# Optimization experiments

Measured on AMD Instinct MI355X. Metric: run time of the kernel, lower is better.

## Reference

```python
import jax, jax.numpy as jnp
import numpy as np

HIDDEN = 3072
N_HEADS = 24
N_KV = 8
HEAD_DIM = HIDDEN // N_HEADS          # 128
ROT = int(HEAD_DIM * 0.75)            # 96 (partial rotary)
OP_SIZE = N_HEADS * HEAD_DIM + 2 * N_KV * HEAD_DIM  # 5120
LORA_R = 256
LORA_SCALE = 512.0 / LORA_R           # 2.0
ROPE_THETA = 10000.0
SCALE = HEAD_DIM ** -0.5


def setup_inputs() -> dict:
    key = jax.random.key(0)
    ks = jax.random.split(key, 8)
    B, S = 2, 2048
    hidden_states = jax.random.normal(ks[0], (B, S, HIDDEN), dtype=jnp.float32)
    position_ids = jnp.arange(B * S, dtype=jnp.int64 if jax.config.jax_enable_x64 else jnp.int32).reshape(B, S)
    w = lambda k, o, i: jax.random.normal(k, (o, i), dtype=jnp.float32) * (i ** -0.5)
    return {
        "hidden_states": hidden_states,
        "Wqkv": w(ks[1], OP_SIZE, HIDDEN),
        "Aqkv": w(ks[2], LORA_R, HIDDEN),
        "Bqkv": w(ks[3], OP_SIZE, LORA_R) * 0.01,
        "Wo": w(ks[4], HIDDEN, N_HEADS * HEAD_DIM),
        "Ao": w(ks[5], LORA_R, N_HEADS * HEAD_DIM),
        "Bo": w(ks[6], HIDDEN, LORA_R) * 0.01,
        "position_ids": position_ids,
    }


def _lora_linear(x, W, A, Bm):
    # base GEMM + low-rank LoRA update, scaling = alpha/r
    return x @ W.T + (x @ A.T) @ Bm.T * LORA_SCALE


def _rotate_half(x):
    h = x.shape[-1] // 2
    return jnp.concatenate((-x[..., h:], x[..., :h]), axis=-1)


def reference(hidden_states, Wqkv, Aqkv, Bqkv, Wo, Ao, Bo, position_ids):
    B, S, _ = hidden_states.shape
    qkv = _lora_linear(hidden_states, Wqkv, Aqkv, Bqkv)  # [B,S,5120]
    q_pos = N_HEADS * HEAD_DIM
    kv_pos = N_KV * HEAD_DIM
    q = qkv[..., :q_pos].reshape(B, S, N_HEADS, HEAD_DIM)
    k = qkv[..., q_pos:q_pos + kv_pos].reshape(B, S, N_KV, HEAD_DIM)
    v = qkv[..., q_pos + kv_pos:].reshape(B, S, N_KV, HEAD_DIM)

    # partial RoPE: cos/sin cache over rotary_ndims=96
    inv_freq = 1.0 / (ROPE_THETA ** (jnp.arange(0, ROT, 2, dtype=jnp.float32) / ROT))  # [48]
    freqs = position_ids.astype(jnp.float32)[..., None] * inv_freq  # [B,S,48]
    emb = jnp.concatenate((freqs, freqs), axis=-1)                   # [B,S,96]
    cos = jnp.cos(emb)[:, :, None, :]  # broadcast over head axis (bsnd)
    sin = jnp.sin(emb)[:, :, None, :]

    def rope(x):
        xr, xp = x[..., :ROT], x[..., ROT:]
        xr = xr * cos + _rotate_half(xr) * sin
        return jnp.concatenate((xr, xp), axis=-1)

    q = rope(q)
    k = rope(k)

    # GQA: repeat kv heads to match query heads
    groups = N_HEADS // N_KV
    k = jnp.repeat(k, groups, axis=2)
    v = jnp.repeat(v, groups, axis=2)

    scores = jnp.einsum('bqhd,bkhd->bhqk', q, k) * SCALE  # [B,H,S,S]
    causal = jnp.tril(jnp.ones((S, S), dtype=bool))
    scores = jnp.where(causal, scores, jnp.finfo(scores.dtype).min)
    probs = jax.nn.softmax(scores, axis=-1)
    attn = jnp.einsum('bhqk,bkhd->bqhd', probs, v).reshape(B, S, N_HEADS * HEAD_DIM)
    return _lora_linear(attn, Wo, Ao, Bo)
```

## Files before the change

### kernel.cpp

```cpp
#include <hip/hip_runtime.h>

typedef unsigned short u16;
typedef unsigned int   u32;

typedef __bf16 bf16_t;
typedef bf16_t bf16x8 __attribute__((ext_vector_type(8)));
typedef float  f32x4  __attribute__((ext_vector_type(4)));
typedef float  f32x16 __attribute__((ext_vector_type(16)));
typedef u16    u16x8  __attribute__((ext_vector_type(8)));
typedef u32    u32x4  __attribute__((ext_vector_type(4)));

__device__ __forceinline__ float bf2f(u16 u) { return __uint_as_float(((u32)u) << 16); }
__device__ __forceinline__ u16 f2bf(float f) {
  u32 u = __float_as_uint(f);
  u32 r = u + 0x7fffu + ((u >> 16) & 1u);
  return (u16)(r >> 16);
}
__device__ __forceinline__ float fast_exp2(float x) { return __builtin_amdgcn_exp2f(x); }

__device__ __forceinline__ void gload_lds16(const u16* g, u16* l) {
  __builtin_amdgcn_global_load_lds(
      (const __attribute__((address_space(1))) void*)g,
      (__attribute__((address_space(3))) void*)l,
      16, 0, 0);
}

#define SBAR0() __builtin_amdgcn_sched_barrier(0)
#define HWBAR() __builtin_amdgcn_s_barrier()

__global__ void k_cast_all(const float* __restrict__ x,  const float* __restrict__ wq,
                           const float* __restrict__ bq, const float* __restrict__ aq,
                           const float* __restrict__ wo, const float* __restrict__ bo,
                           const float* __restrict__ ao,
                           u16* __restrict__ xw, u16* __restrict__ wwq, u16* __restrict__ aqkvb,
                           u16* __restrict__ wwo, u16* __restrict__ aob) {
  const int total = 5177344;
  int i = blockIdx.x * blockDim.x + threadIdx.x;
  const int stride = gridDim.x * blockDim.x;
  for (; i < total; i += stride) {
    const float* src; u16* dst; int r, c8, L, off, sL;
    if (i < 1572864)      { int loc = i;           r = loc / 384; c8 = loc - r * 384; src = x;  dst = xw;    L = 3328; off = 0;    sL = 3072; }
    else if (i < 3538944) { int loc = i - 1572864; r = loc / 384; c8 = loc - r * 384; src = wq; dst = wwq;   L = 3328; off = 0;    sL = 3072; }
    else if (i < 3702784) { int loc = i - 3538944; r = loc >> 5;  c8 = loc & 31;      src = bq; dst = wwq;   L = 3328; off = 3072; sL = 256;  }
    else if (i < 3801088) { int loc = i - 3702784; r = loc / 384; c8 = loc - r * 384; src = aq; dst = aqkvb; L = 3072; off = 0;    sL = 3072; }
    else if (i < 4980736) { int loc = i - 3801088; r = loc / 384; c8 = loc - r * 384; src = wo; dst = wwo;   L = 3328; off = 0;    sL = 3072; }
    else if (i < 5079040) { int loc = i - 4980736; r = loc >> 5;  c8 = loc & 31;      src = bo; dst = wwo;   L = 3328; off = 3072; sL = 256;  }
    else                  { int loc = i - 5079040; r = loc / 384; c8 = loc - r * 384; src = ao; dst = aob;   L = 3072; off = 0;    sL = 3072; }
    const f32x4* p = (const f32x4*)(src + (size_t)r * sL + c8 * 8);
    f32x4 a = p[0], b2 = p[1];
    u16x8 o;
    o[0] = f2bf(a[0]);  o[1] = f2bf(a[1]);  o[2] = f2bf(a[2]);  o[3] = f2bf(a[3]);
    o[4] = f2bf(b2[0]); o[5] = f2bf(b2[1]); o[6] = f2bf(b2[2]); o[7] = f2bf(b2[3]);
    *(u16x8*)(dst + (size_t)r * L + off + c8 * 8) = o;
  }
}

__global__ void k_red4_cast(const float* __restrict__ t4, u16* __restrict__ out,
                            int C8, int L, int off, float scale, size_t plane) {
  const int r  = blockIdx.y;
  const int c8 = blockIdx.x * 64 + threadIdx.x;
  if (c8 >= C8) return;
  size_t base = (size_t)r * (C8 * 8) + c8 * 8;
  float s[8];
#pragma unroll
  for (int j = 0; j < 8; ++j) s[j] = 0.f;
#pragma unroll
  for (int p = 0; p < 4; ++p) {
    const f32x4* q = (const f32x4*)(t4 + p * plane + base);
    f32x4 a = q[0], b = q[1];
    s[0] += a[0]; s[1] += a[1]; s[2] += a[2]; s[3] += a[3];
    s[4] += b[0]; s[5] += b[1]; s[6] += b[2]; s[7] += b[3];
  }
  u16x8 o;
#pragma unroll
  for (int j = 0; j < 8; ++j) o[j] = f2bf(s[j] * scale);
  *(u16x8*)(out + (size_t)r * L + off + c8 * 8) = o;
}

__global__ __launch_bounds__(256) void k_gemm_bt_sk(
    const u16* __restrict__ A, const u16* __restrict__ B, float* __restrict__ C,
    int M, int N, int lda, int ldb, int kc) {
  __shared__ u16 As[64][64 + 8];
  __shared__ u16 Bs[64][64 + 8];
  const int tid   = threadIdx.x;
  const int lane  = tid & 63;
  const int w     = tid >> 6;
  const int wm    = (w >> 1) * 32;
  const int wn    = (w & 1) * 32;
  const int row16 = lane & 15;
  const int quad  = lane >> 4;
  const int m0 = blockIdx.y * 64;
  const int n0 = blockIdx.x * 64;
  const int ldr = tid >> 2;
  const int ldc = (tid & 3) * 16;
  const int z   = blockIdx.z;
  float* Cz = C + (size_t)z * M * N;
  const int kbeg = z * kc, kend = kbeg + kc;

  f32x4 acc[2][2] = {};

  for (int k0 = kbeg; k0 < kend; k0 += 64) {
    const u16* ga = A + (size_t)(m0 + ldr) * lda + (k0 + ldc);
    const u16* gb = B + (size_t)(n0 + ldr) * ldb + (k0 + ldc);
    u16x8 a0 = *(const u16x8*)ga;
    u16x8 a1 = *(const u16x8*)(ga + 8);
    u16x8 b0 = *(const u16x8*)gb;
    u16x8 b1 = *(const u16x8*)(gb + 8);
    __syncthreads();
    *(u16x8*)&As[ldr][ldc]     = a0;
    *(u16x8*)&As[ldr][ldc + 8] = a1;
    *(u16x8*)&Bs[ldr][ldc]     = b0;
    *(u16x8*)&Bs[ldr][ldc + 8] = b1;
    __syncthreads();
#pragma unroll
    for (int kk = 0; kk < 64; kk += 32) {
      bf16x8 af0 = *(const bf16x8*)&As[wm + row16][kk + quad * 8];
      bf16x8 af1 = *(const bf16x8*)&As[wm + 16 + row16][kk + quad * 8];
      bf16x8 bg0 = *(const bf16x8*)&Bs[wn + row16][kk + quad * 8];
      bf16x8 bg1 = *(const bf16x8*)&Bs[wn + 16 + row16][kk + quad * 8];
      acc[0][0] = __builtin_amdgcn_mfma_f32_16x16x32_bf16(af0, bg0, acc[0][0], 0, 0, 0);
      acc[0][1] = __builtin_amdgcn_mfma_f32_16x16x32_bf16(af0, bg1, acc[0][1], 0, 0, 0);
      acc[1][0] = __builtin_amdgcn_mfma_f32_16x16x32_bf16(af1, bg0, acc[1][0], 0, 0, 0);
      acc[1][1] = __builtin_amdgcn_mfma_f32_16x16x32_bf16(af1, bg1, acc[1][1], 0, 0, 0);
    }
  }
#pragma unroll
  for (int tm = 0; tm < 2; ++tm)
#pragma unroll
    for (int tn = 0; tn < 2; ++tn) {
      int gm = m0 + wm + tm * 16 + quad * 4;
      int gn = n0 + wn + tn * 16 + row16;
#pragma unroll
      for (int r = 0; r < 4; ++r)
        Cz[(size_t)(gm + r) * N + gn] = acc[tm][tn][r];
    }
}

__device__ __forceinline__ void stage_half(
    int H, int nt4,
    const u16* __restrict__ A, const u16* __restrict__ B, int S,
    int m0, int n0, u16* AsB, u16* BsB,
    int w, int rowin, int colsw) {
  if (H >= nt4) return;
  const int t = H >> 2, slot = H & 3;
  const int half = slot & 1;
  const u16* G = (slot < 2) ? A : B;
  const int r0 = (slot < 2) ? m0 : n0;
  u16* lds = ((slot < 2) ? AsB : BsB) + (t & 1) * 16384 + half * 8192;
  const int k0 = t * 64;
#pragma unroll
  for (int i = 0; i < 2; ++i) {
    const int chunk = w * 2 + i;
    const int row = half * 128 + chunk * 8 + rowin;
    gload_lds16(G + (size_t)(r0 + row) * S + k0 + colsw, lds + chunk * 512);
  }
}

__device__ __forceinline__ bf16x8 frag_ld(const u16* base, int row, int c16) {
  return *(const bf16x8*)(base + row * 64 + ((c16 ^ (row & 7)) << 3));
}

template <int RB>
__device__ __forceinline__ void gemm256_group(
    int k, int nt,
    const u16* __restrict__ A, const u16* __restrict__ B, int S,
    int m0, int n0, u16* AsB, u16* BsB,
    int wr, int wc, int row16, int quad, int w, int rowin, int colsw,
    f32x4 (&acc)[8][4]) {
  const u16* Ab = AsB + RB * 16384;
  const u16* Bb = BsB + RB * 16384;
  const int nt4 = nt * 4;
  bf16x8 a0[4][2], a1[4][2], b0[2][2], b1[2][2];

#pragma unroll
  for (int mf = 0; mf < 4; ++mf)
#pragma unroll
    for (int kk = 0; kk < 2; ++kk)
      a0[mf][kk] = frag_ld(Ab, wr * 128 + mf * 16 + row16, kk * 4 + quad);
#pragma unroll
  for (int nf = 0; nf < 2; ++nf)
#pragma unroll
    for (int kk = 0; kk < 2; ++kk)
      b0[nf][kk] = frag_ld(Bb, wc * 64 + nf * 16 + row16, kk * 4 + quad);
  stage_half(4 * k + 5, nt4, A, B, S, m0, n0, AsB, BsB, w, rowin, colsw);
  SBAR0(); HWBAR(); SBAR0();
  __builtin_amdgcn_s_setprio(1);
#pragma unroll
  for (int mf = 0; mf < 4; ++mf)
#pragma unroll
    for (int nf = 0; nf < 2; ++nf)
#pragma unroll
      for (int kk = 0; kk < 2; ++kk)
        acc[mf][nf] = __builtin_amdgcn_mfma_f32_16x16x32_bf16(a0[mf][kk], b0[nf][kk], acc[mf][nf], 0, 0, 0);
  __builtin_amdgcn_s_setprio(0);
  SBAR0(); HWBAR(); SBAR0();

#pragma unroll
  for (int nf = 0; nf < 2; ++nf)
#pragma unroll
    for (int kk = 0; kk < 2; ++kk)
      b1[nf][kk] = frag_ld(Bb, wc * 64 + 32 + nf * 16 + row16, kk * 4 + quad);
  stage_half(4 * k + 6, nt4, A, B, S, m0, n0, AsB, BsB, w, rowin, colsw);
  SBAR0(); HWBAR(); SBAR0();
  __builtin_amdgcn_s_setprio(1);
#pragma unroll
  for (int mf = 0; mf < 4; ++mf)
#pragma unroll
    for (int nf = 0; nf < 2; ++nf)
#pragma unroll
      for (int kk = 0; kk < 2; ++kk)
        acc[mf][2 + nf] = __builtin_amdgcn_mfma_f32_16x16x32_bf16(a0[mf][kk], b1[nf][kk], acc[mf][2 + nf], 0, 0, 0);
  __builtin_amdgcn_s_setprio(0);
  SBAR0(); HWBAR(); SBAR0();

#pragma unroll
  for (int mf = 0; mf < 4; ++mf)
#pragma unroll
    for (int kk = 0; kk < 2; ++kk)
      a1[mf][kk] = frag_ld(Ab, wr * 128 + 64 + mf * 16 + row16, kk * 4 + quad);
  stage_half(4 * k + 7, nt4, A, B, S, m0, n0, AsB, BsB, w, rowin, colsw);
  SBAR0(); HWBAR(); SBAR0();
  __builtin_amdgcn_s_setprio(1);
#pragma unroll
  for (int mf = 0; mf < 4; ++mf)
#pragma unroll
    for (int nf = 0; nf < 2; ++nf)
#pragma unroll
      for (int kk = 0; kk < 2; ++kk)
        acc[4 + mf][nf] = __builtin_amdgcn_mfma_f32_16x16x32_bf16(a1[mf][kk], b0[nf][kk], acc[4 + mf][nf], 0, 0, 0);
  __builtin_amdgcn_s_setprio(0);
  SBAR0(); HWBAR(); SBAR0();

  stage_half(4 * k + 8, nt4, A, B, S, m0, n0, AsB, BsB, w, rowin, colsw);
  SBAR0();
  if (k < nt - 2) { asm volatile("s_waitcnt vmcnt(2)" ::: "memory"); }
  else            { asm volatile("s_waitcnt vmcnt(0)" ::: "memory"); }
  HWBAR(); SBAR0();
  __builtin_amdgcn_s_setprio(1);
#pragma unroll
  for (int mf = 0; mf < 4; ++mf)
#pragma unroll
    for (int nf = 0; nf < 2; ++nf)
#pragma unroll
      for (int kk = 0; kk < 2; ++kk)
        acc[4 + mf][2 + nf] = __builtin_amdgcn_mfma_f32_16x16x32_bf16(a1[mf][kk], b1[nf][kk], acc[4 + mf][2 + nf], 0, 0, 0);
  __builtin_amdgcn_s_setprio(0);
  SBAR0(); HWBAR(); SBAR0();
}

template <int ATOMIC>
__device__ __forceinline__ void gemm256_run(
    const u16* __restrict__ A, const u16* __restrict__ B, int S, int nt,
    int m0, int n0, float* __restrict__ C, int ldc, int cn0,
    u16* As, u16* Bs) {
  const int tid   = threadIdx.x;
  const int lane  = tid & 63;
  const int w     = tid >> 6;
  const int wr    = w >> 2;
  const int wc    = w & 3;
  const int row16 = lane & 15;
  const int quad  = lane >> 4;
  const int rowin = lane >> 3;
  const int colsw = ((lane & 7) ^ (lane >> 3)) << 3;

  f32x4 acc[8][4] = {};

#pragma unroll
  for (int H = 0; H < 5; ++H)
    stage_half(H, nt * 4, A, B, S, m0, n0, As, Bs, w, rowin, colsw);
  asm volatile("s_waitcnt vmcnt(2)" ::: "memory");
  HWBAR(); SBAR0();

  int k = 0;
  for (; k + 1 < nt; k += 2) {
    gemm256_group<0>(k,     nt, A, B, S, m0, n0, As, Bs, wr, wc, row16, quad, w, rowin, colsw, acc);
    gemm256_group<1>(k + 1, nt, A, B, S, m0, n0, As, Bs, wr, wc, row16, quad, w, rowin, colsw, acc);
  }
  if (k < nt)
    gemm256_group<0>(k, nt, A, B, S, m0, n0, As, Bs, wr, wc, row16, quad, w, rowin, colsw, acc);

#pragma unroll
  for (int mi = 0; mi < 8; ++mi) {
    const int gm = m0 + wr * 128 + mi * 16 + quad * 4;
#pragma unroll
    for (int nj = 0; nj < 4; ++nj) {
      const int gn = cn0 + wc * 64 + nj * 16 + row16;
#pragma unroll
      for (int r = 0; r < 4; ++r) {
        if (ATOMIC) atomicAdd(&C[(size_t)(gm + r) * ldc + gn], acc[mi][nj][r]);
        else        C[(size_t)(gm + r) * ldc + gn] = acc[mi][nj][r];
      }
    }
  }
}

__global__ __launch_bounds__(512, 2) void k_gemm256(
    const u16* __restrict__ A, const u16* __restrict__ B, float* __restrict__ C,
    int M, int N, int K) {
  __shared__ u16 As[2 * 16384];
  __shared__ u16 Bs[2 * 16384];
  const int nwg = (int)gridDim.x;
  const int bid = (int)blockIdx.x;
  const int xcd = bid & 7, rest = bid >> 3;
  const int qq = nwg >> 3, rr = nwg & 7;
  const int wg = (xcd < rr ? xcd * (qq + 1) : rr * (qq + 1) + (xcd - rr) * qq) + rest;
  const int nbx = N >> 8;
  const int m0 = (wg / nbx) << 8;
  const int n0 = (wg % nbx) << 8;
  gemm256_run<0>(A, B, K, K >> 6, m0, n0, C, N, n0, As, Bs);
}

__global__ __launch_bounds__(512, 2) void k_gemm256_qkv(
    const u16* __restrict__ A, const u16* __restrict__ B,
    float* __restrict__ Cqk, float* __restrict__ Cv) {
  __shared__ u16 As[2 * 16384];
  __shared__ u16 Bs[2 * 16384];
  const int bid = (int)blockIdx.x;
  const int xcd = bid & 7, rest = bid >> 3;
  const int wg = xcd * 32 + rest;
  const int m0 = (wg >> 4) << 8;
  const int n0 = (wg & 15) << 8;
  gemm256_run<0>(A, B, 3328, 52, m0, n0, Cqk, 4096, n0, As, Bs);
  __syncthreads();
  const int m  = bid & 15;
  const int nv = (bid >> 4) & 3;
  const int kc = bid >> 6;
  const u16* At = A + kc * 832;
  const u16* Bt = B + (size_t)4096 * 3328 + kc * 832;
  gemm256_run<1>(At, Bt, 3328, 13, m * 256, nv * 256, Cv, 1024, nv * 256, As, Bs);
}

__global__ void k_rope_tab(const int* __restrict__ pos_ids, float* __restrict__ tab,
                           int* __restrict__ ctr) {
  if (blockIdx.x == 0 && threadIdx.x == 0) *ctr = 0;
  const int t = threadIdx.x;
  const int r = blockIdx.x * 4 + t / 48;
  const int j = t % 48;
  const float pos = (float)pos_ids[r];
  float invf = powf(10000.0f, -(float)j * (1.0f / 48.0f));
  float e = pos * invf;
  tab[(size_t)r * 96 + j]      = cosf(e);
  tab[(size_t)r * 96 + 48 + j] = sinf(e);
}

__global__ void k_rope_v(const float* __restrict__ qk, const float* __restrict__ vsrc,
                         const float* __restrict__ tab,
                         u16* __restrict__ qb, u16* __restrict__ kb, u16* __restrict__ vtg) {
  const int y = blockIdx.y;
  const int d = threadIdx.x;
  if (y < 32) {
    const int r  = blockIdx.x;
    const int hh = y;
    const float* src;
    if (hh < 24) src = qk + (size_t)r * 4096 + hh * 128;
    else         src = qk + (size_t)r * 4096 + 3072 + (hh - 24) * 128;
    float x = src[d];
    float outv;
    if (d >= 96) {
      outv = x;
    } else {
      int j = (d < 48) ? d : d - 48;
      float c  = tab[(size_t)r * 96 + j];
      float sn = tab[(size_t)r * 96 + 48 + j];
      if (d < 48) outv = x * c - src[d + 48] * sn;
      else        outv = x * c + src[d - 48] * sn;
    }
    u16 o = f2bf(outv);
    if (hh < 24) qb[((size_t)r * 24 + hh) * 128 + d] = o;
    else         kb[((size_t)r * 8 + (hh - 24)) * 128 + d] = o;
  } else {
    const int bk = blockIdx.x >> 8;
    const int kg = blockIdx.x & 255;
    const int b = bk >> 3, kvh = bk & 7;
    const float* src = vsrc + (size_t)(b * 2048 + kg * 8) * 1024 + kvh * 128 + d;
    u16x8 pack;
#pragma unroll
    for (int t = 0; t < 8; ++t) pack[t] = f2bf(src[(size_t)t * 1024]);
    *(u16x8*)(vtg + ((size_t)bk * 128 + d) * 2048 + kg * 8) = pack;
  }
}

#define NJOBS 768

__global__ __launch_bounds__(256) void k_attn_mfma(
    const u16* __restrict__ qb, const u16* __restrict__ kb, const u16* __restrict__ vtg,
    u16* __restrict__ attnw, int* __restrict__ ctr) {
  __shared__ u16 Ks0[8192], Ks1[8192];
  __shared__ u16 Vt0[8192], Vt1[8192];
  __shared__ int s_job;

  const int tid  = threadIdx.x;
  const int lane = tid & 63;
  const int w    = tid >> 6;
  const int l31  = lane & 31;
  const int hi   = lane >> 5;
  const int r7   = lane & 7;
  const float C1 = 0.08838834764831845f * 1.4426950408889634f;

  for (;;) {
    if (tid == 0) s_job = atomicAdd(ctr, 1);
    __syncthreads();
    const int j = s_job;
    if (j >= NJOBS) return;

    const int qt  = 15 - (j / 48);
    const int bh  = j % 48;
    const int b   = bh / 24;
    const int h   = bh % 24;
    const int kvh = h / 3;
    const int q0  = qt * 128;
    const int qrow = q0 + w * 32 + l31;

    const u16* qrb = qb + (((size_t)(b * 2048 + qrow)) * 24 + h) * 128;
    bf16x8 qf[8];
#pragma unroll
    for (int kk = 0; kk < 8; ++kk) qf[kk] = *(const bf16x8*)(qrb + kk * 16 + hi * 8);

    const u16* kbbase = kb + ((size_t)(b * 2048) * 8 + kvh) * 128;
    const u16* vtbase = vtg + (size_t)(b * 8 + kvh) * 128 * 2048;

    f32x16 o32[4] = {};
    float m_st = -INFINITY, l_st = 0.f;
    const int ntile = 2 * qt + 2;

#define STAGE_K(Kd, KB0)                                                        \
  { _Pragma("unroll") for (int i = 0; i < 4; ++i) {                             \
      const int c = w * 4 + i;                                                  \
      const int rowk = 4 * c + (lane >> 4);                                     \
      gload_lds16(kbbase + (size_t)((KB0) + rowk) * 1024 +                      \
                      (((lane & 15) ^ (rowk & 7)) << 3),                        \
                  (Kd) + c * 512); } }
#define STAGE_V(Vd, KB0)                                                        \
  { _Pragma("unroll") for (int i = 0; i < 4; ++i) {                             \
      const int c = w * 4 + i;                                                  \
      const int rowv = 8 * c + (lane >> 3);                                     \
      gload_lds16(vtbase + (size_t)rowv * 2048 + (KB0) +                        \
                      (((lane & 7) ^ (rowv & 7)) << 3),                         \
                  (Vd) + c * 512); } }

    STAGE_K(Ks0, 0);
    STAGE_V(Vt0, 0);

    for (int t = 0; t < ntile; ++t) {
      const int kb0 = t * 64;
      const u16* Kc = (t & 1) ? Ks1 : Ks0;
      const u16* Vc = (t & 1) ? Vt1 : Vt0;

      asm volatile("s_waitcnt vmcnt(0)" ::: "memory");
      SBAR0(); HWBAR(); SBAR0();
      if (t + 1 < ntile) {
        u16* Kn = (t & 1) ? Ks0 : Ks1;
        u16* Vn = (t & 1) ? Vt0 : Vt1;
        STAGE_K(Kn, kb0 + 64);
        STAGE_V(Vn, kb0 + 64);
      }
      SBAR0();

      f32x16 s0 = {}, s1 = {};
      __builtin_amdgcn_s_setprio(1);
#pragma unroll
      for (int kk = 0; kk < 8; ++kk) {
        bf16x8 kf0 = *(const bf16x8*)&Kc[l31 * 128 + (((2 * kk + hi) ^ r7) << 3)];
        s0 = __builtin_amdgcn_mfma_f32_32x32x16_bf16(kf0, qf[kk], s0, 0, 0, 0);
        bf16x8 kf1 = *(const bf16x8*)&Kc[(32 + l31) * 128 + (((2 * kk + hi) ^ ((32 + l31) & 7)) << 3)];
        s1 = __builtin_amdgcn_mfma_f32_32x32x16_bf16(kf1, qf[kk], s1, 0, 0, 0);
      }
      __builtin_amdgcn_s_setprio(0);

      if (kb0 >= q0) {
#pragma unroll
        for (int r = 0; r < 16; ++r) {
          const int crow = (r & 3) + 8 * (r >> 2) + 4 * hi;
          if (kb0 + crow > qrow)      s0[r] = -INFINITY;
          if (kb0 + 32 + crow > qrow) s1[r] = -INFINITY;
        }
      }

      float tm[8];
#pragma unroll
      for (int r = 0; r < 8; ++r)
        tm[r] = fmaxf(fmaxf(s0[r], s0[r + 8]), fmaxf(s1[r], s1[r + 8]));
#pragma unroll
      for (int st = 4; st >= 1; st >>= 1)
#pragma unroll
        for (int r = 0; r < 4; ++r)
          if (r < st) tm[r] = fmaxf(tm[r], tm[r + st]);
      float mx = fmaxf(tm[0], __shfl_xor(tm[0], 32));

      const bool skip = __all((mx - m_st) * C1 <= 8.0f);
      if (!skip) {
        const float mnew = fmaxf(m_st, mx);
        const float alpha = fast_exp2((m_st - mnew) * C1);
        l_st *= alpha;
#pragma unroll
        for (int dt = 0; dt < 4; ++dt)
#pragma unroll
          for (int r = 0; r < 16; ++r) o32[dt][r] *= alpha;
        m_st = mnew;
      }
      const float mc = m_st * C1;
      float ts[8];
#pragma unroll
      for (int r = 0; r < 16; ++r) {
        s0[r] = fast_exp2(__builtin_fmaf(s0[r], C1, -mc));
        s1[r] = fast_exp2(__builtin_fmaf(s1[r], C1, -mc));
      }
#pragma unroll
      for (int r = 0; r < 8; ++r) ts[r] = (s0[r] + s0[r + 8]) + (s1[r] + s1[r + 8]);
#pragma unroll
      for (int st = 4; st >= 1; st >>= 1)
#pragma unroll
        for (int r = 0; r < 4; ++r)
          if (r < st) ts[r] += ts[r + st];
      l_st += ts[0] + __shfl_xor(ts[0], 32);

#pragma unroll
      for (int kt = 0; kt < 2; ++kt) {
        const f32x16& sv = kt ? s1 : s0;
        u32 pk[8];
#pragma unroll
        for (int i = 0; i < 8; ++i)
          asm("v_cvt_pk_bf16_f32 %0, %1, %2"
              : "=v"(pk[i]) : "v"(sv[2 * i]), "v"(sv[2 * i + 1]));
        u32 e0 = __shfl_xor(hi ? pk[0] : pk[2], 32);
        u32 e1 = __shfl_xor(hi ? pk[1] : pk[3], 32);
        u32 e2 = __shfl_xor(hi ? pk[4] : pk[6], 32);
        u32 e3 = __shfl_xor(hi ? pk[5] : pk[7], 32);
        u32x4 w0, w1;
        w0[0] = hi ? e0 : pk[0]; w0[1] = hi ? e1 : pk[1];
        w0[2] = hi ? pk[2] : e0; w0[3] = hi ? pk[3] : e1;
        w1[0] = hi ? e2 : pk[4]; w1[1] = hi ? e3 : pk[5];
        w1[2] = hi ? pk[6] : e2; w1[3] = hi ? pk[7] : e3;
        bf16x8 pb0 = __builtin_bit_cast(bf16x8, w0);
        bf16x8 pb1 = __builtin_bit_cast(bf16x8, w1);
        __builtin_amdgcn_s_setprio(1);
#pragma unroll
        for (int dt = 0; dt < 4; ++dt) {
          const int vrow = dt * 32 + l31;
          bf16x8 vf0 = *(const bf16x8*)&Vc[vrow * 64 + (((2 * (2 * kt) + hi) ^ (vrow & 7)) << 3)];
          o32[dt] = __builtin_amdgcn_mfma_f32_32x32x16_bf16(vf0, pb0, o32[dt], 0, 0, 0);
          bf16x8 vf1 = *(const bf16x8*)&Vc[vrow * 64 + (((2 * (2 * kt + 1) + hi) ^ (vrow & 7)) << 3)];
          o32[dt] = __builtin_amdgcn_mfma_f32_32x32x16_bf16(vf1, pb1, o32[dt], 0, 0, 0);
        }
        __builtin_amdgcn_s_setprio(0);
      }
    }

    __syncthreads();
    const float inv = 1.0f / l_st;
    u16* scr = ((w < 2) ? Ks0 : Ks1) + (w & 1) * 4096;
#pragma unroll
    for (int dt = 0; dt < 4; ++dt)
#pragma unroll
      for (int r = 0; r < 16; ++r) {
        const int d = 32 * dt + (r & 3) + 8 * (r >> 2) + 4 * hi;
        const int slot = (d >> 3) ^ (l31 & 7);
        scr[l31 * 128 + slot * 8 + (d & 7)] = f2bf(o32[dt][r] * inv);
      }
    const int q32r = lane >> 1, part = lane & 1;
    const size_t grow = ((size_t)(b * 2048 + q0 + w * 32 + q32r)) * 3328 + (size_t)h * 128;
#pragma unroll
    for (int c = 0; c < 8; ++c) {
      const int d0 = part * 64 + c * 8;
      const int s2 = (d0 >> 3) ^ (q32r & 7);
      *(u16x8*)(attnw + grow + d0) = *(const u16x8*)&scr[q32r * 128 + s2 * 8];
    }
  }
}

#define OFF_XW    ((size_t)0)
#define OFF_WWQ   ((size_t)27262976)
#define OFF_AQKVB ((size_t)61341696)
#define OFF_WWO   ((size_t)62914560)
#define OFF_AOB   ((size_t)83361792)
#define OFF_QKV   ((size_t)84934656)
#define OFF_QKVV  (OFF_QKV + (size_t)67108864)
#define OFF_TA4   OFF_QKV
#define OFF_QB    OFF_XW
#define OFF_KB    OFF_WWQ
#define OFF_VTG   (OFF_WWQ + (size_t)8388608)
#define OFF_RTAB  (OFF_WWQ + (size_t)16777216)
#define OFF_CTR   (OFF_WWQ + (size_t)18350080)
#define OFF_ATTNW OFF_QKV
#define OFF_TO4   (OFF_QKV + (size_t)27262976)

extern "C" void kernel_launch(void* const* d_in, const int* in_sizes, int n_in,
                              void* d_out, int out_size, void* d_ws, size_t ws_size,
                              hipStream_t stream) {
  const float* x    = (const float*)d_in[0];
  const float* Wqkv = (const float*)d_in[1];
  const float* Aqkv = (const float*)d_in[2];
  const float* Bqkv = (const float*)d_in[3];
  const float* Wo   = (const float*)d_in[4];
  const float* Ao   = (const float*)d_in[5];
  const float* Bo   = (const float*)d_in[6];
  const int*   pos  = (const int*)d_in[7];
  float* out = (float*)d_out;
  char* ws = (char*)d_ws;

  u16* xw    = (u16*)(ws + OFF_XW);
  u16* wwq   = (u16*)(ws + OFF_WWQ);
  u16* aqkvb = (u16*)(ws + OFF_AQKVB);
  u16* wwo   = (u16*)(ws + OFF_WWO);
  u16* aob   = (u16*)(ws + OFF_AOB);
  float* qk  = (float*)(ws + OFF_QKV);
  float* qv  = (float*)(ws + OFF_QKVV);
  float* tA4 = (float*)(ws + OFF_TA4);
  u16* qb    = (u16*)(ws + OFF_QB);
  u16* kb    = (u16*)(ws + OFF_KB);
  u16* vtg   = (u16*)(ws + OFF_VTG);
  float* rtab = (float*)(ws + OFF_RTAB);
  int* ctr   = (int*)(ws + OFF_CTR);
  u16* attnw = (u16*)(ws + OFF_ATTNW);
  float* tO4 = (float*)(ws + OFF_TO4);

  k_cast_all<<<2048, 256, 0, stream>>>(x, Wqkv, Bqkv, Aqkv, Wo, Bo, Ao,
                                       xw, wwq, aqkvb, wwo, aob);

  k_gemm_bt_sk<<<dim3(4, 64, 4), 256, 0, stream>>>(xw, aqkvb, tA4, 4096, 256, 3328, 3072, 768);
  k_red4_cast<<<dim3(1, 4096), 64, 0, stream>>>(tA4, xw, 32, 3328, 3072, 2.f, (size_t)4096 * 256);

  hipMemsetAsync(qv, 0, (size_t)4096 * 1024 * 4, stream);
  k_gemm256_qkv<<<dim3(256), 512, 0, stream>>>(xw, wwq, qk, qv);

  k_rope_tab<<<dim3(1024), 192, 0, stream>>>(pos, rtab, ctr);
  k_rope_v<<<dim3(4096, 33), 128, 0, stream>>>(qk, qv, rtab, qb, kb, vtg);

  k_attn_mfma<<<dim3(512), 256, 0, stream>>>(qb, kb, vtg, attnw, ctr);

  k_gemm_bt_sk<<<dim3(4, 64, 4), 256, 0, stream>>>(attnw, aob, tO4, 4096, 256, 3328, 3072, 768);
  k_red4_cast<<<dim3(1, 4096), 64, 0, stream>>>(tO4, attnw, 32, 3328, 3072, 2.f, (size_t)4096 * 256);

  k_gemm256<<<dim3((3072 / 256) * (4096 / 256)), 512, 0, stream>>>(attnw, wwo, out, 4096, 3072, 3328);
}
```

Baseline: 684.2 us.

## Replace atomic V split-K with two bf16 partial buffers summed in rope kernel

```diff
diff --git a/kernel.cpp b/kernel.cpp
--- a/kernel.cpp
+++ b/kernel.cpp
@@ -248,10 +248,10 @@
   SBAR0(); HWBAR(); SBAR0();
 }
 
-template <int ATOMIC>
+template <int BF16OUT>
 __device__ __forceinline__ void gemm256_run(
     const u16* __restrict__ A, const u16* __restrict__ B, int S, int nt,
-    int m0, int n0, float* __restrict__ C, int ldc, int cn0,
+    int m0, int n0, void* __restrict__ Cp, int ldc, int cn0,
     u16* As, u16* Bs) {
   const int tid   = threadIdx.x;
   const int lane  = tid & 63;
@@ -287,8 +287,8 @@
       const int gn = cn0 + wc * 64 + nj * 16 + row16;
 #pragma unroll
       for (int r = 0; r < 4; ++r) {
-        if (ATOMIC) atomicAdd(&C[(size_t)(gm + r) * ldc + gn], acc[mi][nj][r]);
-        else        C[(size_t)(gm + r) * ldc + gn] = acc[mi][nj][r];
+        if (BF16OUT) ((u16*)Cp)[(size_t)(gm + r) * ldc + gn] = f2bf(acc[mi][nj][r]);
+        else         ((float*)Cp)[(size_t)(gm + r) * ldc + gn] = acc[mi][nj][r];
       }
     }
   }
@@ -312,7 +312,7 @@
 
 __global__ __launch_bounds__(512, 2) void k_gemm256_qkv(
     const u16* __restrict__ A, const u16* __restrict__ B,
-    float* __restrict__ Cqk, float* __restrict__ Cv) {
+    float* __restrict__ Cqk, u16* __restrict__ Cvp) {
   __shared__ u16 As[2 * 16384];
   __shared__ u16 Bs[2 * 16384];
   const int bid = (int)blockIdx.x;
@@ -321,13 +321,15 @@
   const int m0 = (wg >> 4) << 8;
   const int n0 = (wg & 15) << 8;
   gemm256_run<0>(A, B, 3328, 52, m0, n0, Cqk, 4096, n0, As, Bs);
+  if (bid >= 128) return;
   __syncthreads();
   const int m  = bid & 15;
   const int nv = (bid >> 4) & 3;
   const int kc = bid >> 6;
-  const u16* At = A + kc * 832;
-  const u16* Bt = B + (size_t)4096 * 3328 + kc * 832;
-  gemm256_run<1>(At, Bt, 3328, 13, m * 256, nv * 256, Cv, 1024, nv * 256, As, Bs);
+  const u16* At = A + kc * 1664;
+  const u16* Bt = B + (size_t)4096 * 3328 + kc * 1664;
+  gemm256_run<1>(At, Bt, 3328, 26, m * 256, nv * 256,
+                 Cvp + (size_t)kc * 4096 * 1024, 1024, nv * 256, As, Bs);
 }
 
 __global__ void k_rope_tab(const int* __restrict__ pos_ids, float* __restrict__ tab,
@@ -343,7 +345,7 @@
   tab[(size_t)r * 96 + 48 + j] = sinf(e);
 }
 
-__global__ void k_rope_v(const float* __restrict__ qk, const float* __restrict__ vsrc,
+__global__ void k_rope_v(const float* __restrict__ qk, const u16* __restrict__ vp,
                          const float* __restrict__ tab,
                          u16* __restrict__ qb, u16* __restrict__ kb, u16* __restrict__ vtg) {
   const int y = blockIdx.y;
@@ -372,10 +374,12 @@
     const int bk = blockIdx.x >> 8;
     const int kg = blockIdx.x & 255;
     const int b = bk >> 3, kvh = bk & 7;
-    const float* src = vsrc + (size_t)(b * 2048 + kg * 8) * 1024 + kvh * 128 + d;
+    const u16* s0 = vp + (size_t)(b * 2048 + kg * 8) * 1024 + kvh * 128 + d;
+    const u16* s1 = s0 + (size_t)4096 * 1024;
     u16x8 pack;
 #pragma unroll
-    for (int t = 0; t < 8; ++t) pack[t] = f2bf(src[(size_t)t * 1024]);
+    for (int t = 0; t < 8; ++t)
+      pack[t] = f2bf(bf2f(s0[(size_t)t * 1024]) + bf2f(s1[(size_t)t * 1024]));
     *(u16x8*)(vtg + ((size_t)bk * 128 + d) * 2048 + kg * 8) = pack;
   }
 }
@@ -574,7 +578,7 @@
 #define OFF_WWO   ((size_t)62914560)
 #define OFF_AOB   ((size_t)83361792)
 #define OFF_QKV   ((size_t)84934656)
-#define OFF_QKVV  (OFF_QKV + (size_t)67108864)
+#define OFF_CVP   (OFF_QKV + (size_t)67108864)
 #define OFF_TA4   OFF_QKV
 #define OFF_QB    OFF_XW
 #define OFF_KB    OFF_WWQ
@@ -604,7 +608,7 @@
   u16* wwo   = (u16*)(ws + OFF_WWO);
   u16* aob   = (u16*)(ws + OFF_AOB);
   float* qk  = (float*)(ws + OFF_QKV);
-  float* qv  = (float*)(ws + OFF_QKVV);
+  u16* cvp   = (u16*)(ws + OFF_CVP);
   float* tA4 = (float*)(ws + OFF_TA4);
   u16* qb    = (u16*)(ws + OFF_QB);
   u16* kb    = (u16*)(ws + OFF_KB);
@@ -620,11 +624,10 @@
   k_gemm_bt_sk<<<dim3(4, 64, 4), 256, 0, stream>>>(xw, aqkvb, tA4, 4096, 256, 3328, 3072, 768);
   k_red4_cast<<<dim3(1, 4096), 64, 0, stream>>>(tA4, xw, 32, 3328, 3072, 2.f, (size_t)4096 * 256);
 
-  hipMemsetAsync(qv, 0, (size_t)4096 * 1024 * 4, stream);
-  k_gemm256_qkv<<<dim3(256), 512, 0, stream>>>(xw, wwq, qk, qv);
+  k_gemm256_qkv<<<dim3(256), 512, 0, stream>>>(xw, wwq, qk, cvp);
 
   k_rope_tab<<<dim3(1024), 192, 0, stream>>>(pos, rtab, ctr);
-  k_rope_v<<<dim3(4096, 33), 128, 0, stream>>>(qk, qv, rtab, qb, kb, vtg);
+  k_rope_v<<<dim3(4096, 33), 128, 0, stream>>>(qk, cvp, rtab, qb, kb, vtg);
 
   k_attn_mfma<<<dim3(512), 256, 0, stream>>>(qb, kb, vtg, attnw, ctr);
 
```

After: 652.0 us. 1.05x faster.
